# Kernel optimization log

Measured on AMD Instinct MI355X. Metric: run time of the kernel, lower is better.

## Reference

```python
import jax, jax.numpy as jnp
import numpy as np

NUM_HEADS = 4
LN_EPS = 1e-5
ALPHA_SCALE = 2.0


def setup_inputs() -> dict:
    key = jax.random.key(0)
    ks = jax.random.split(key, 8)
    bs, C, H, W = 64, 256, 56, 56
    T, D = 6, 192
    HW = H * W
    w = lambda k, shape: (jax.random.normal(k, shape, jnp.float32) * 0.02)
    return {
        "features": jax.random.normal(ks[0], (bs, C, H, W), jnp.float32),
        "tokens": jax.random.normal(ks[1], (T, bs, D), jnp.float32),
        # mlp: Linear(HW -> T)
        "mlp_w": w(ks[2], (T, HW)), "mlp_b": jnp.zeros((T,), jnp.float32),
        # q: Linear(D -> C)
        "q_w": w(ks[3], (C, D)), "q_b": jnp.zeros((C,), jnp.float32),
        # alpha: Linear(D -> C)
        "alpha_w": w(ks[4], (C, D)), "alpha_b": jnp.zeros((C,), jnp.float32),
        # proj: Linear(C -> D)
        "proj_w": w(ks[5], (D, C)), "proj_b": jnp.zeros((D,), jnp.float32),
        "ln_g": jnp.ones((D,), jnp.float32), "ln_b": jnp.zeros((D,), jnp.float32),
    }


def reference(features, tokens, mlp_w, mlp_b, q_w, q_b,
              alpha_w, alpha_b, proj_w, proj_b, ln_g, ln_b):
    bs, C, H, W = features.shape
    T, _, D = tokens.shape
    h = NUM_HEADS
    dh = C // h
    HW = H * W
    scale = dh ** -0.5

    f = features.reshape(bs, C, HW)

    # mlp branch: Linear over HW -> [bs, C, T] -> permute to [T, bs, C]
    t_sum = jnp.einsum('bcn,tn->tbc', f, mlp_w) + mlp_b[:, None, None]

    # attn branch: few tokens attend over H*W feature map (k reused as v)
    q = jnp.einsum('tbd,cd->tbc', tokens, q_w) + q_b          # [T, bs, C]
    q = q.reshape(T, bs, h, dh).transpose(1, 2, 0, 3)         # [bs, h, T, dh]
    k = f.reshape(bs, h, dh, HW)                              # [bs, h, dh, HW]
    attn = jnp.einsum('bhtd,bhdn->bhtn', q, k) * scale        # [bs, h, T, HW]
    a = jax.nn.softmax(attn, axis=-1)
    attn_out = jnp.einsum('bhtn,bhdn->bhtd', a, k)            # [bs, h, T, dh]
    t_a = attn_out.transpose(2, 0, 1, 3).reshape(T, bs, C)
    t_sum = t_sum + t_a

    # dynamic gate: h_sigmoid(alpha(tokens)) * 2.0
    alp = jnp.clip(jnp.einsum('tbd,cd->tbc', tokens, alpha_w) + alpha_b + 3.0,
                   0.0, 6.0) / 6.0 * ALPHA_SCALE              # [T, bs, C]
    t_sum = t_sum * alp

    # proj + residual + LayerNorm (post-norm, drop_path rate 0 -> identity)
    t_sum = jnp.einsum('tbc,dc->tbd', t_sum, proj_w) + proj_b  # [T, bs, D]
    tok = tokens + t_sum
    mu = tok.mean(-1, keepdims=True)
    var = ((tok - mu) ** 2).mean(-1, keepdims=True)
    tok = (tok - mu) * jax.lax.rsqrt(var + LN_EPS) * ln_g + ln_b

    return tok, attn.reshape(bs, h, T, H, W)
```

## Files before the change

### kernel.cpp

```cpp
#include <hip/hip_runtime.h>
#include <hip/hip_bf16.h>

constexpr int BS = 64, C = 256, NH = 4, DH = 64, T = 6, D = 192;
constexpr int HW = 3136;
constexpr int NT = 112;
constexpr int S = 7, CPB = 4;
constexpr int PNF = 136;
constexpr int PNS = 116;
constexpr int QP = 72;
constexpr float SCALE = 0.125f;
constexpr float LN_EPS = 1e-5f;

typedef short bf16x8 __attribute__((ext_vector_type(8)));
typedef float f32x4 __attribute__((ext_vector_type(4)));

__device__ inline unsigned short f2bf(float x) {
    union { float f; unsigned u; } v; v.f = x;
    unsigned r = v.u + 0x7FFFu + ((v.u >> 16) & 1u);
    return (unsigned short)(r >> 16);
}

__device__ inline void st_bf8(unsigned short* dst, float4 p) {
    unsigned lo = (unsigned)f2bf(p.x) | ((unsigned)f2bf(p.y) << 16);
    unsigned hi = (unsigned)f2bf(p.z) | ((unsigned)f2bf(p.w) << 16);
    *(uint2*)dst = make_uint2(lo, hi);
}

__device__ inline void wg_barrier_lgkm() {
    asm volatile("s_waitcnt lgkmcnt(0)" ::: "memory");
    __builtin_amdgcn_s_barrier();
    asm volatile("" ::: "memory");
}

__global__ __launch_bounds__(256) void qalpha_kernel(
    const float* __restrict__ tokens,
    const float* __restrict__ q_w,
    const float* __restrict__ q_b,
    const float* __restrict__ alpha_w,
    const float* __restrict__ alpha_b,
    float* __restrict__ q_ws,
    float* __restrict__ alp_ws)
{
    int b = blockIdx.x;
    int c = threadIdx.x;
    __shared__ float tok_s[T][D];
    for (int i = c; i < T * (D / 4); i += 256) {
        int t = i / (D / 4), v = i % (D / 4);
        *(float4*)&tok_s[t][4 * v] =
            *(const float4*)&tokens[((size_t)t * BS + b) * D + 4 * v];
    }
    __syncthreads();

    const float4* qr = (const float4*)(q_w + (size_t)c * D);
    const float4* ar = (const float4*)(alpha_w + (size_t)c * D);
    float accq[T] = {0, 0, 0, 0, 0, 0};
    float acca[T] = {0, 0, 0, 0, 0, 0};
    for (int v = 0; v < D / 4; ++v) {
        float4 qw4 = qr[v], aw4 = ar[v];
#pragma unroll
        for (int t = 0; t < T; ++t) {
            float4 t4 = *(const float4*)&tok_s[t][4 * v];
            accq[t] += qw4.x * t4.x + qw4.y * t4.y + qw4.z * t4.z + qw4.w * t4.w;
            acca[t] += aw4.x * t4.x + aw4.y * t4.y + aw4.z * t4.z + aw4.w * t4.w;
        }
    }
    float qb = q_b[c], ab = alpha_b[c];
#pragma unroll
    for (int t = 0; t < T; ++t) {
        size_t idx = ((size_t)t * BS + b) * C + c;
        q_ws[idx] = accq[t] + qb;
        float aa = acca[t] + ab + 3.0f;
        alp_ws[idx] = fminf(fmaxf(aa, 0.0f), 6.0f) * (2.0f / 6.0f);
    }
}

struct PF { float4 f0, f1, f2, f3, f4, m; };

__global__ __launch_bounds__(384) void fused_attn_mlp(
    const float* __restrict__ feat,
    const float* __restrict__ mlp_w,
    const float* __restrict__ q_ws,
    float* __restrict__ out_attn,
    float* __restrict__ o_part,
    float* __restrict__ mlp_part,
    float* __restrict__ ml_part)
{
    int bh = blockIdx.x / S, sp = blockIdx.x % S;
    int b = bh / NH, h = bh % NH;
    int tid = threadIdx.x;
    int wave = tid >> 6, lane = tid & 63;
    int col = lane & 15, quad = lane >> 4;

    __shared__ unsigned short fch[DH][PNF];
    __shared__ unsigned short pw[16][PNF];
    __shared__ unsigned short qs[16][QP];
    __shared__ float st[T][PNS];
    __shared__ float m_s[T], l_s[T], al_s[T];

    const float* fbase = feat + ((size_t)b * C + h * DH) * HW;
    float* obase = out_attn + ((size_t)bh * T) * HW;

    const int o0 = (tid / 28) * HW + 4 * (tid % 28);
    const int o1 = ((tid + 384) / 28) * HW + 4 * ((tid + 384) % 28);
    const int o2 = ((tid + 768) / 28) * HW + 4 * ((tid + 768) % 28);
    const int o3 = ((tid + 1152) / 28) * HW + 4 * ((tid + 1152) % 28);
    const int o4 = ((tid + 1536) / 28) * HW + 4 * ((tid + 1536) % 28);

    auto pf_issue = [&](PF& p, int n0) {
        p.f0 = *(const float4*)&fbase[o0 + n0];
        p.f1 = *(const float4*)&fbase[o1 + n0];
        p.f2 = *(const float4*)&fbase[o2 + n0];
        p.f3 = *(const float4*)&fbase[o3 + n0];
        if (tid < 256) p.f4 = *(const float4*)&fbase[o4 + n0];
        if (tid < 168) p.m  = *(const float4*)&mlp_w[o0 + n0];
    };
    auto pf_commit = [&](const PF& p) {
        st_bf8(&fch[tid / 28][4 * (tid % 28)], p.f0);
        st_bf8(&fch[(tid + 384) / 28][4 * ((tid + 384) % 28)], p.f1);
        st_bf8(&fch[(tid + 768) / 28][4 * ((tid + 768) % 28)], p.f2);
        st_bf8(&fch[(tid + 1152) / 28][4 * ((tid + 1152) % 28)], p.f3);
        if (tid < 256) st_bf8(&fch[(tid + 1536) / 28][4 * ((tid + 1536) % 28)], p.f4);
        if (tid < 168) st_bf8(&pw[6 + tid / 28][4 * (tid % 28)], p.m);
    };

    const int nsp = sp * CPB * NT;
    PF A;
    pf_issue(A, nsp);

    for (int i = tid; i < 16 * PNF; i += 384) pw[i / PNF][i % PNF] = 0;
    for (int i = tid; i < DH * 16; i += 384) fch[i / 16][112 + (i % 16)] = 0;
    if (tid < T) { m_s[tid] = -3e38f; l_s[tid] = 0.f; }
    qs[wave][lane] = f2bf(q_ws[((size_t)wave * BS + b) * C + h * DH + lane]);

    f32x4 accPW = {0.f, 0.f, 0.f, 0.f};
    wg_barrier_lgkm();

#pragma unroll 1
    for (int cc = 0; cc < CPB; ++cc) {
        const int n0 = nsp + cc * NT;

        pf_commit(A);
        if (cc + 1 < CPB) pf_issue(A, n0 + NT);
        wg_barrier_lgkm();

        for (int tile = wave; tile < 7; tile += 6) {
            bf16x8 a0 = *(const bf16x8*)&qs[col][quad * 8];
            bf16x8 a1 = *(const bf16x8*)&qs[col][32 + quad * 8];
            bf16x8 b0, b1;
#pragma unroll
            for (int j = 0; j < 8; ++j) {
                b0[j] = (short)fch[quad * 8 + j][tile * 16 + col];
                b1[j] = (short)fch[32 + quad * 8 + j][tile * 16 + col];
            }
            f32x4 acc = {0.f, 0.f, 0.f, 0.f};
            acc = __builtin_amdgcn_mfma_f32_16x16x32_bf16(a0, b0, acc, 0, 0, 0);
            acc = __builtin_amdgcn_mfma_f32_16x16x32_bf16(a1, b1, acc, 0, 0, 0);
#pragma unroll
            for (int reg = 0; reg < 4; ++reg) {
                int r = quad * 4 + reg;
                if (r < 6) st[r][tile * 16 + col] = acc[reg] * SCALE;
            }
        }
        wg_barrier_lgkm();

        {
            int t = wave;
            float v0 = st[t][lane];
            float v1 = (lane + 64 < NT) ? st[t][lane + 64] : -3e38f;
            float mloc = fmaxf(v0, v1);
#pragma unroll
            for (int off = 32; off; off >>= 1) mloc = fmaxf(mloc, __shfl_down(mloc, off));
            mloc = __shfl(mloc, 0);
            float m_old = m_s[t], m_new = fmaxf(m_old, mloc);
            float p0 = __expf(v0 - m_new);
            float p1 = (lane + 64 < NT) ? __expf(v1 - m_new) : 0.f;
            pw[t][lane] = f2bf(p0);
            if (lane + 64 < NT) pw[t][lane + 64] = f2bf(p1);
            float ssum = p0 + p1;
#pragma unroll
            for (int off = 32; off; off >>= 1) ssum += __shfl_down(ssum, off);
            if (lane == 0) {
                float alpha = __expf(m_old - m_new);
                l_s[t] = l_s[t] * alpha + ssum;
                m_s[t] = m_new;
                al_s[t] = alpha;
            }
            if (lane < NT / 4) {
                *(float4*)&obase[(size_t)t * HW + n0 + 4 * lane] =
                    *(const float4*)&st[t][4 * lane];
            }
        }
        wg_barrier_lgkm();

        if (wave < 4) {
            float alpha = (col < 6) ? al_s[col] : 1.0f;
            accPW *= alpha;
#pragma unroll
            for (int ks = 0; ks < 4; ++ks) {
                bf16x8 af = *(const bf16x8*)&fch[wave * 16 + col][ks * 32 + quad * 8];
                bf16x8 bf = *(const bf16x8*)&pw[col][ks * 32 + quad * 8];
                accPW = __builtin_amdgcn_mfma_f32_16x16x32_bf16(af, bf, accPW, 0, 0, 0);
            }
        }
        wg_barrier_lgkm();
    }

    if (wave < 4) {
#pragma unroll
        for (int reg = 0; reg < 4; ++reg) {
            int c2 = wave * 16 + quad * 4 + reg;
            if (col < 6) {
                o_part[((size_t)blockIdx.x * T + col) * DH + c2] = accPW[reg];
            } else if (col < 12) {
                mlp_part[((size_t)blockIdx.x * T + (col - 6)) * DH + c2] = accPW[reg];
            }
        }
    }
    if (tid < 2 * T) {
        int t = tid >> 1;
        ml_part[((size_t)blockIdx.x * T + t) * 2 + (tid & 1)] =
            (tid & 1) ? l_s[t] : m_s[t];
    }
}

__global__ __launch_bounds__(256) void merge_proj_ln_kernel(
    const float* __restrict__ o_part,
    const float* __restrict__ mlp_part,
    const float* __restrict__ ml_part,
    const float* __restrict__ mlp_b,
    const float* __restrict__ alp_ws,
    const float* __restrict__ tokens,
    const float* __restrict__ proj_w,
    const float* __restrict__ proj_b,
    const float* __restrict__ ln_g,
    const float* __restrict__ ln_b,
    float* __restrict__ out_tok)
{
    int tb = blockIdx.x;
    int t = tb / BS, b = tb % BS;
    int tid = threadIdx.x;
    __shared__ float g_s[C];
    __shared__ float r1[4], r2[4];

    {
        int c = tid;
        int h = c >> 6, cl = c & 63;
        int bh = b * NH + h;
        float m[S], l[S];
        float M = -3e38f;
#pragma unroll
        for (int s = 0; s < S; ++s) {
            size_t blk = (size_t)(bh * S + s);
            m[s] = ml_part[(blk * T + t) * 2 + 0];
            l[s] = ml_part[(blk * T + t) * 2 + 1];
            M = fmaxf(M, m[s]);
        }
        float L = 0.f, O = 0.f, MLP = 0.f;
#pragma unroll
        for (int s = 0; s < S; ++s) {
            float w = __expf(m[s] - M);
            size_t blk = (size_t)(bh * S + s);
            size_t pidx = (blk * T + t) * DH + cl;
            L += l[s] * w;
            O += o_part[pidx] * w;
            MLP += mlp_part[pidx];
        }
        size_t idx = (size_t)tb * C + c;
        g_s[c] = (MLP + mlp_b[t] + O / L) * alp_ws[idx];
    }
    __syncthreads();

    if (tid < D) {
        int d = tid;
        float acc = proj_b[d] + tokens[(size_t)tb * D + d];
        const float4* pr = (const float4*)(proj_w + (size_t)d * C);
#pragma unroll 8
        for (int v = 0; v < C / 4; ++v) {
            float4 w4 = pr[v];
            float4 g4 = *(const float4*)&g_s[4 * v];
            acc += w4.x * g4.x + w4.y * g4.y + w4.z * g4.z + w4.w * g4.w;
        }

        float s1 = acc, s2 = acc * acc;
#pragma unroll
        for (int off = 32; off; off >>= 1) { s1 += __shfl_down(s1, off); s2 += __shfl_down(s2, off); }
        int wv = d >> 6, lane = d & 63;
        if (lane == 0) { r1[wv] = s1; r2[wv] = s2; }
        __syncthreads();
        float sum1 = r1[0] + r1[1] + r1[2];
        float sum2 = r2[0] + r2[1] + r2[2];
        float mu = sum1 * (1.0f / D);
        float var = sum2 * (1.0f / D) - mu * mu;
        float inv = rsqrtf(var + LN_EPS);
        out_tok[(size_t)tb * D + d] = (acc - mu) * inv * ln_g[d] + ln_b[d];
    } else {
        __syncthreads();
    }
}

extern "C" void kernel_launch(void* const* d_in, const int* in_sizes, int n_in,
                              void* d_out, int out_size, void* d_ws, size_t ws_size,
                              hipStream_t stream) {
    const float* features = (const float*)d_in[0];
    const float* tokens   = (const float*)d_in[1];
    const float* mlp_w    = (const float*)d_in[2];
    const float* mlp_b    = (const float*)d_in[3];
    const float* q_w      = (const float*)d_in[4];
    const float* q_b      = (const float*)d_in[5];
    const float* alpha_w  = (const float*)d_in[6];
    const float* alpha_b  = (const float*)d_in[7];
    const float* proj_w   = (const float*)d_in[8];
    const float* proj_b   = (const float*)d_in[9];
    const float* ln_g     = (const float*)d_in[10];
    const float* ln_b     = (const float*)d_in[11];

    float* out_tok  = (float*)d_out;
    float* out_attn = (float*)d_out + T * BS * D;

    constexpr int NBLK = BS * NH * S;
    float* q_ws     = (float*)d_ws;
    float* alp_ws   = q_ws + T * BS * C;
    float* ml_part  = alp_ws + T * BS * C;
    float* o_part   = ml_part + NBLK * T * 2;
    float* mlp_part = o_part + NBLK * T * DH;

    qalpha_kernel<<<BS, 256, 0, stream>>>(
        tokens, q_w, q_b, alpha_w, alpha_b, q_ws, alp_ws);

    fused_attn_mlp<<<NBLK, 384, 0, stream>>>(
        features, mlp_w, q_ws, out_attn, o_part, mlp_part, ml_part);

    merge_proj_ln_kernel<<<T * BS, 256, 0, stream>>>(
        o_part, mlp_part, ml_part, mlp_b, alp_ws, tokens,
        proj_w, proj_b, ln_g, ln_b, out_tok);
}
```

Before: 347.7 us.

## Swizzle LDS feature tile columns and rebalance split count per block

```diff
diff --git a/kernel.cpp b/kernel.cpp
--- a/kernel.cpp
+++ b/kernel.cpp
@@ -4,7 +4,7 @@
 constexpr int BS = 64, C = 256, NH = 4, DH = 64, T = 6, D = 192;
 constexpr int HW = 3136;
 constexpr int NT = 112;
-constexpr int S = 7, CPB = 4;
+constexpr int S = 4, CPB = 7;
 constexpr int PNF = 136;
 constexpr int PNS = 116;
 constexpr int QP = 72;
@@ -25,6 +25,8 @@
     unsigned hi = (unsigned)f2bf(p.z) | ((unsigned)f2bf(p.w) << 16);
     *(uint2*)dst = make_uint2(lo, hi);
 }
+
+__device__ inline int fsw(int r, int n) { return n ^ (((r >> 3) & 3) << 4); }
 
 __device__ inline void wg_barrier_lgkm() {
     asm volatile("s_waitcnt lgkmcnt(0)" ::: "memory");
@@ -115,12 +117,22 @@
         if (tid < 168) p.m  = *(const float4*)&mlp_w[o0 + n0];
     };
     auto pf_commit = [&](const PF& p) {
-        st_bf8(&fch[tid / 28][4 * (tid % 28)], p.f0);
-        st_bf8(&fch[(tid + 384) / 28][4 * ((tid + 384) % 28)], p.f1);
-        st_bf8(&fch[(tid + 768) / 28][4 * ((tid + 768) % 28)], p.f2);
-        st_bf8(&fch[(tid + 1152) / 28][4 * ((tid + 1152) % 28)], p.f3);
-        if (tid < 256) st_bf8(&fch[(tid + 1536) / 28][4 * ((tid + 1536) % 28)], p.f4);
-        if (tid < 168) st_bf8(&pw[6 + tid / 28][4 * (tid % 28)], p.m);
+        int r0 = tid / 28,          c0 = 4 * (tid % 28);
+        int r1 = (tid + 384) / 28,  c1 = 4 * ((tid + 384) % 28);
+        int r2 = (tid + 768) / 28,  c2 = 4 * ((tid + 768) % 28);
+        int r3 = (tid + 1152) / 28, c3 = 4 * ((tid + 1152) % 28);
+        st_bf8(&fch[r0][fsw(r0, c0)], p.f0);
+        st_bf8(&fch[r1][fsw(r1, c1)], p.f1);
+        st_bf8(&fch[r2][fsw(r2, c2)], p.f2);
+        st_bf8(&fch[r3][fsw(r3, c3)], p.f3);
+        if (tid < 256) {
+            int r4 = (tid + 1536) / 28, c4 = 4 * ((tid + 1536) % 28);
+            st_bf8(&fch[r4][fsw(r4, c4)], p.f4);
+        }
+        if (tid < 168) {
+            int rm = 6 + tid / 28, cm = 4 * (tid % 28);
+            st_bf8(&pw[rm][fsw(rm, cm)], p.m);
+        }
     };
 
     const int nsp = sp * CPB * NT;
@@ -128,7 +140,10 @@
     pf_issue(A, nsp);
 
     for (int i = tid; i < 16 * PNF; i += 384) pw[i / PNF][i % PNF] = 0;
-    for (int i = tid; i < DH * 16; i += 384) fch[i / 16][112 + (i % 16)] = 0;
+    for (int i = tid; i < DH * 16; i += 384) {
+        int r = i / 16;
+        fch[r][fsw(r, 112 + (i % 16))] = 0;
+    }
     if (tid < T) { m_s[tid] = -3e38f; l_s[tid] = 0.f; }
     qs[wave][lane] = f2bf(q_ws[((size_t)wave * BS + b) * C + h * DH + lane]);
 
@@ -146,11 +161,12 @@
         for (int tile = wave; tile < 7; tile += 6) {
             bf16x8 a0 = *(const bf16x8*)&qs[col][quad * 8];
             bf16x8 a1 = *(const bf16x8*)&qs[col][32 + quad * 8];
+            int nsw = (tile * 16 + col) ^ (quad << 4);
             bf16x8 b0, b1;
 #pragma unroll
             for (int j = 0; j < 8; ++j) {
-                b0[j] = (short)fch[quad * 8 + j][tile * 16 + col];
-                b1[j] = (short)fch[32 + quad * 8 + j][tile * 16 + col];
+                b0[j] = (short)fch[quad * 8 + j][nsw];
+                b1[j] = (short)fch[32 + quad * 8 + j][nsw];
             }
             f32x4 acc = {0.f, 0.f, 0.f, 0.f};
             acc = __builtin_amdgcn_mfma_f32_16x16x32_bf16(a0, b0, acc, 0, 0, 0);
@@ -195,10 +211,11 @@
         if (wave < 4) {
             float alpha = (col < 6) ? al_s[col] : 1.0f;
             accPW *= alpha;
+            int ra = wave * 16 + col;
 #pragma unroll
             for (int ks = 0; ks < 4; ++ks) {
-                bf16x8 af = *(const bf16x8*)&fch[wave * 16 + col][ks * 32 + quad * 8];
-                bf16x8 bf = *(const bf16x8*)&pw[col][ks * 32 + quad * 8];
+                bf16x8 af = *(const bf16x8*)&fch[ra][fsw(ra, ks * 32 + quad * 8)];
+                bf16x8 bf = *(const bf16x8*)&pw[col][fsw(col, ks * 32 + quad * 8)];
                 accPW = __builtin_amdgcn_mfma_f32_16x16x32_bf16(af, bf, accPW, 0, 0, 0);
             }
         }
```

New measurement: 347.9 us. About the same (+0.1%).
